# Optimization experiments

Hardware: AMD Instinct MI355X
Metric: run time of the kernel (lower is better)

Reference implementation:

```python
import jax, jax.numpy as jnp
import numpy as np

B, L, E, D1, D2 = 256, 128, 64, 512, 512


def setup_inputs() -> dict:
    key = jax.random.key(0)
    k1, k2, k3, kw = jax.random.split(key, 4)
    tensor1 = jax.random.normal(k1, (B, L, D1), dtype=jnp.float32)
    tensor2 = jax.random.normal(k2, (B, L, D2), dtype=jnp.float32)
    parameters_index = jax.random.randint(k3, (B,), 0, E, dtype=jnp.int32)
    # xavier_uniform with relu gain: gain*sqrt(6/(fan_in+fan_out)),
    # torch fan for [E,D1,D2]: fan_in = D1*D2, fan_out = E*D2
    gain = float(np.sqrt(2.0))
    bound = gain * float(np.sqrt(6.0 / (D1 * D2 + E * D2)))
    weights = jax.random.uniform(kw, (E, D1, D2), minval=-bound, maxval=bound, dtype=jnp.float32)
    return {"tensor1": tensor1, "tensor2": tensor2, "parameters_index": parameters_index, "weights": weights}


def reference(tensor1, tensor2, parameters_index, weights):
    # gather per-batch weight matrix [B, D1, D2], then bilinear form x1^T W x2
    w = weights[parameters_index]  # [B, D1, D2]
    # equals: sum over i,j of tensor1[b,l,i] * w[b,i,j] * tensor2[b,l,j] -> [B, L]
    return jnp.einsum('bli,bij,blj->bl', tensor1, w, tensor2)
```

## Files before the change

### kernel.cpp

```cpp
#include <hip/hip_runtime.h>
#include <stdint.h>

#define NB 256
#define NL 128
#define ND1 512
#define ND2 512

#define BI 128
#define BK 64
#define NKT (ND2 / BK)
#define LDST 72

typedef float float4_t __attribute__((ext_vector_type(4)));
typedef __bf16 bf16x8_t __attribute__((ext_vector_type(8)));
typedef unsigned short ushort4_t __attribute__((ext_vector_type(4)));
typedef unsigned short ushort8_t __attribute__((ext_vector_type(8)));

__device__ __forceinline__ unsigned short f2bf(float f) {
    unsigned int u = __float_as_uint(f);
    u += 0x7FFFu + ((u >> 16) & 1u);
    return (unsigned short)(u >> 16);
}

__global__ __launch_bounds__(256, 4) void pdot_kernel(
    const float* __restrict__ t1, const float* __restrict__ t2,
    const int* __restrict__ pidx, const float* __restrict__ wgt,
    float* __restrict__ out)
{
    __shared__ unsigned short sA[NL * LDST];
    __shared__ unsigned short sB[BI * LDST];

    const int g  = blockIdx.x;
    const int b  = g & (NB - 1);
    const int it = g >> 8;
    const int i0 = it * BI;

    const int t  = threadIdx.x;
    const int wv = t >> 6;
    const int ln = t & 63;
    const int nh = ln & 15;
    const int qd = ln >> 4;

    const int e = pidx[b];
    const float* aPtr  = t2  + (size_t)b * (NL * ND2);
    const float* bPtr  = wgt + (size_t)e * (ND1 * ND2) + (size_t)i0 * ND2;
    const float* t1p   = t1  + (size_t)b * (NL * ND1) + i0;

    float4_t acc[2][8];
    #pragma unroll
    for (int i = 0; i < 2; ++i)
        #pragma unroll
        for (int j = 0; j < 8; ++j) {
            float4_t z = {0.f, 0.f, 0.f, 0.f};
            acc[i][j] = z;
        }

    const int s_row = t >> 4;
    const int s_kq  = (t & 15) * 4;

    for (int kt = 0; kt < NKT; ++kt) {
        const int k0 = kt * BK;

        #pragma unroll
        for (int p = 0; p < 8; ++p) {
            const int row = p * 16 + s_row;
            float4_t va = *(const float4_t*)(aPtr + (size_t)row * ND2 + (k0 + s_kq));
            float4_t vb = *(const float4_t*)(bPtr + (size_t)row * ND2 + (k0 + s_kq));
            ushort4_t ua, ub;
            ua.x = f2bf(va.x); ua.y = f2bf(va.y); ua.z = f2bf(va.z); ua.w = f2bf(va.w);
            ub.x = f2bf(vb.x); ub.y = f2bf(vb.y); ub.z = f2bf(vb.z); ub.w = f2bf(vb.w);
            *(ushort4_t*)(&sA[row * LDST + s_kq]) = ua;
            *(ushort4_t*)(&sB[row * LDST + s_kq]) = ub;
        }

        __syncthreads();

        #pragma unroll
        for (int ks = 0; ks < 2; ++ks) {
            const int kf = ks * 32 + qd * 8;
            bf16x8_t af[2];
            bf16x8_t bfr[8];
            #pragma unroll
            for (int ms = 0; ms < 2; ++ms) {
                const int row = wv * 32 + ms * 16 + nh;
                af[ms] = __builtin_bit_cast(bf16x8_t, *(ushort8_t*)(&sA[row * LDST + kf]));
            }
            #pragma unroll
            for (int ns = 0; ns < 8; ++ns) {
                const int nr = ns * 16 + nh;
                bfr[ns] = __builtin_bit_cast(bf16x8_t, *(ushort8_t*)(&sB[nr * LDST + kf]));
            }
            #pragma unroll
            for (int ms = 0; ms < 2; ++ms)
                #pragma unroll
                for (int ns = 0; ns < 8; ++ns)
                    acc[ms][ns] = __builtin_amdgcn_mfma_f32_16x16x32_bf16(af[ms], bfr[ns], acc[ms][ns], 0, 0, 0);
        }

        __syncthreads();
    }

    #pragma unroll
    for (int ms = 0; ms < 2; ++ms) {
        #pragma unroll
        for (int r = 0; r < 4; ++r) {
            const int row = wv * 32 + ms * 16 + qd * 4 + r;
            float ps = 0.f;
            #pragma unroll
            for (int ns = 0; ns < 8; ++ns) {
                const float tv = t1p[(size_t)row * ND1 + ns * 16 + nh];
                ps += acc[ms][ns][r] * tv;
            }
            ps += __shfl_xor(ps, 1);
            ps += __shfl_xor(ps, 2);
            ps += __shfl_xor(ps, 4);
            ps += __shfl_xor(ps, 8);
            if (nh == 0) atomicAdd(&out[b * NL + row], ps);
        }
    }
}

extern "C" void kernel_launch(void* const* d_in, const int* in_sizes, int n_in,
                              void* d_out, int out_size, void* d_ws, size_t ws_size,
                              hipStream_t stream)
{
    const float* t1  = (const float*)d_in[0];
    const float* t2  = (const float*)d_in[1];
    const int* pidx  = (const int*)d_in[2];
    const float* wgt = (const float*)d_in[3];
    float* out = (float*)d_out;

    hipMemsetAsync(out, 0, (size_t)out_size * sizeof(float), stream);
    pdot_kernel<<<dim3(NB * (ND1 / BI)), dim3(256), 0, stream>>>(t1, t2, pidx, wgt, out);
}
```

Before: 243.4 us.

## Register-prefetch next K tile of global loads to overlap with MFMA compute

Adds software pipelining: global float4 loads for tile kt+2 are issued into registers while tile kt+1 is converted and stored to LDS, hiding global latency behind the MFMA loop. Barriers become explicit s_barrier with sched_barrier fences and a manual lgkmcnt wait. The MFMA inner loop is also reordered to interleave B-fragment loads with MFMAs. Occupancy hint drops from 4 to 3 waves per SIMD to make room for the 64 extra prefetch registers.

After: 217.5 us. 1.12x faster.

```diff
diff --git a/kernel.cpp b/kernel.cpp
--- a/kernel.cpp
+++ b/kernel.cpp
@@ -22,7 +22,13 @@
     return (unsigned short)(u >> 16);
 }
 
-__global__ __launch_bounds__(256, 4) void pdot_kernel(
+__device__ __forceinline__ ushort4_t cvt4(float4_t v) {
+    ushort4_t u;
+    u.x = f2bf(v.x); u.y = f2bf(v.y); u.z = f2bf(v.z); u.w = f2bf(v.w);
+    return u;
+}
+
+__global__ __launch_bounds__(256, 3) void pdot_kernel(
     const float* __restrict__ t1, const float* __restrict__ t2,
     const int* __restrict__ pidx, const float* __restrict__ wgt,
     float* __restrict__ out)
@@ -57,47 +63,72 @@
 
     const int s_row = t >> 4;
     const int s_kq  = (t & 15) * 4;
+    const size_t sOff = (size_t)s_row * ND2 + s_kq;
+
+    float4_t pa[8], pb[8];
+
+    #pragma unroll
+    for (int p = 0; p < 8; ++p) {
+        pa[p] = *(const float4_t*)(aPtr + sOff + (size_t)p * (16 * ND2));
+        pb[p] = *(const float4_t*)(bPtr + sOff + (size_t)p * (16 * ND2));
+    }
+    #pragma unroll
+    for (int p = 0; p < 8; ++p) {
+        const int row = p * 16 + s_row;
+        *(ushort4_t*)(&sA[row * LDST + s_kq]) = cvt4(pa[p]);
+        *(ushort4_t*)(&sB[row * LDST + s_kq]) = cvt4(pb[p]);
+    }
+    #pragma unroll
+    for (int p = 0; p < 8; ++p) {
+        pa[p] = *(const float4_t*)(aPtr + sOff + BK + (size_t)p * (16 * ND2));
+        pb[p] = *(const float4_t*)(bPtr + sOff + BK + (size_t)p * (16 * ND2));
+    }
+    __builtin_amdgcn_sched_barrier(0);
+    asm volatile("s_waitcnt lgkmcnt(0)" ::: "memory");
+    __builtin_amdgcn_sched_barrier(0);
+    __builtin_amdgcn_s_barrier();
+    __builtin_amdgcn_sched_barrier(0);
 
     for (int kt = 0; kt < NKT; ++kt) {
-        const int k0 = kt * BK;
-
-        #pragma unroll
-        for (int p = 0; p < 8; ++p) {
-            const int row = p * 16 + s_row;
-            float4_t va = *(const float4_t*)(aPtr + (size_t)row * ND2 + (k0 + s_kq));
-            float4_t vb = *(const float4_t*)(bPtr + (size_t)row * ND2 + (k0 + s_kq));
-            ushort4_t ua, ub;
-            ua.x = f2bf(va.x); ua.y = f2bf(va.y); ua.z = f2bf(va.z); ua.w = f2bf(va.w);
-            ub.x = f2bf(vb.x); ub.y = f2bf(vb.y); ub.z = f2bf(vb.z); ub.w = f2bf(vb.w);
-            *(ushort4_t*)(&sA[row * LDST + s_kq]) = ua;
-            *(ushort4_t*)(&sB[row * LDST + s_kq]) = ub;
-        }
-
-        __syncthreads();
-
         #pragma unroll
         for (int ks = 0; ks < 2; ++ks) {
             const int kf = ks * 32 + qd * 8;
-            bf16x8_t af[2];
-            bf16x8_t bfr[8];
-            #pragma unroll
-            for (int ms = 0; ms < 2; ++ms) {
-                const int row = wv * 32 + ms * 16 + nh;
-                af[ms] = __builtin_bit_cast(bf16x8_t, *(ushort8_t*)(&sA[row * LDST + kf]));
-            }
+            const int ra = wv * 32 + nh;
+            bf16x8_t af0 = __builtin_bit_cast(bf16x8_t, *(ushort8_t*)(&sA[(ra     ) * LDST + kf]));
+            bf16x8_t af1 = __builtin_bit_cast(bf16x8_t, *(ushort8_t*)(&sA[(ra + 16) * LDST + kf]));
             #pragma unroll
             for (int ns = 0; ns < 8; ++ns) {
-                const int nr = ns * 16 + nh;
-                bfr[ns] = __builtin_bit_cast(bf16x8_t, *(ushort8_t*)(&sB[nr * LDST + kf]));
+                bf16x8_t bv = __builtin_bit_cast(bf16x8_t, *(ushort8_t*)(&sB[(ns * 16 + nh) * LDST + kf]));
+                acc[0][ns] = __builtin_amdgcn_mfma_f32_16x16x32_bf16(af0, bv, acc[0][ns], 0, 0, 0);
+                acc[1][ns] = __builtin_amdgcn_mfma_f32_16x16x32_bf16(af1, bv, acc[1][ns], 0, 0, 0);
             }
-            #pragma unroll
-            for (int ms = 0; ms < 2; ++ms)
-                #pragma unroll
-                for (int ns = 0; ns < 8; ++ns)
-                    acc[ms][ns] = __builtin_amdgcn_mfma_f32_16x16x32_bf16(af[ms], bfr[ns], acc[ms][ns], 0, 0, 0);
         }
 
-        __syncthreads();
+        if (kt < NKT - 1) {
+            __builtin_amdgcn_sched_barrier(0);
+            __builtin_amdgcn_s_barrier();
+            __builtin_amdgcn_sched_barrier(0);
+
+            #pragma unroll
+            for (int p = 0; p < 8; ++p) {
+                const int row = p * 16 + s_row;
+                *(ushort4_t*)(&sA[row * LDST + s_kq]) = cvt4(pa[p]);
+                *(ushort4_t*)(&sB[row * LDST + s_kq]) = cvt4(pb[p]);
+            }
+            if (kt < NKT - 2) {
+                const size_t k0 = (size_t)(kt + 2) * BK;
+                #pragma unroll
+                for (int p = 0; p < 8; ++p) {
+                    pa[p] = *(const float4_t*)(aPtr + sOff + k0 + (size_t)p * (16 * ND2));
+                    pb[p] = *(const float4_t*)(bPtr + sOff + k0 + (size_t)p * (16 * ND2));
+                }
+            }
+            __builtin_amdgcn_sched_barrier(0);
+            asm volatile("s_waitcnt lgkmcnt(0)" ::: "memory");
+            __builtin_amdgcn_sched_barrier(0);
+            __builtin_amdgcn_s_barrier();
+            __builtin_amdgcn_sched_barrier(0);
+        }
     }
 
     #pragma unroll
```
